# Optimization experiments

Measured on AMD Instinct MI355X. Metric: run time of the kernel, lower is better.

The kernel has to match this reference:

```python
import jax, jax.numpy as jnp
import numpy as np

NUM_GRAPHS = 512


def setup_inputs() -> dict:
    key = jax.random.key(0)
    k1, k2, k3, k4, k5, k6, k7 = jax.random.split(key, 7)
    N, E, D_IN, D_H = 100000, 3200000, 384, 64
    x_sem = jax.random.normal(k1, (N, D_IN), dtype=jnp.float32)
    edge_index = jax.random.randint(k2, (2, E), 0, N, dtype=jnp.int64)
    batch_index = jnp.sort(jax.random.randint(k3, (N,), 0, NUM_GRAPHS, dtype=jnp.int64))
    # GCNConv params: linear (no bias) + separate bias; classifier Linear(D_H, 1)
    W_gcn = jax.random.normal(k4, (D_IN, D_H), dtype=jnp.float32) / np.sqrt(D_IN)
    b_gcn = jnp.zeros((D_H,), dtype=jnp.float32)
    W_cls = jax.random.normal(k5, (D_H, 1), dtype=jnp.float32) / np.sqrt(D_H)
    b_cls = jnp.zeros((1,), dtype=jnp.float32)
    return {"x_sem": x_sem, "edge_index": edge_index, "batch_index": batch_index,
            "W_gcn": W_gcn, "b_gcn": b_gcn, "W_cls": W_cls, "b_cls": b_cls}


def reference(x_sem, edge_index, batch_index, W_gcn, b_gcn, W_cls, b_cls):
    N = x_sem.shape[0]
    # GCNConv: add self-loops, symmetric deg^{-1/2} A deg^{-1/2} normalization
    loop = jnp.arange(N, dtype=edge_index.dtype)
    src = jnp.concatenate([edge_index[0], loop])  # message source (x_j)
    dst = jnp.concatenate([edge_index[1], loop])  # aggregation target
    deg = jax.ops.segment_sum(jnp.ones_like(dst, dtype=x_sem.dtype), dst, num_segments=N)
    deg_inv_sqrt = jnp.where(deg > 0, jax.lax.rsqrt(jnp.maximum(deg, 1.0)), 0.0)
    norm = deg_inv_sqrt[src] * deg_inv_sqrt[dst]  # [E+N]
    h = x_sem @ W_gcn                                       # [N, D_H] project first (cheaper)
    msg = h[src] * norm[:, None]                            # gather + scale
    agg = jax.ops.segment_sum(msg, dst, num_segments=N) + b_gcn
    h = jax.nn.relu(agg)
    # global_add_pool over sorted batch_index
    z_graph = jax.ops.segment_sum(h, batch_index, num_segments=NUM_GRAPHS)  # [G, D_H]
    logits = z_graph @ W_cls + b_cls                        # [G, 1]
    return jnp.squeeze(logits, axis=-1)                     # [G]
```

## Files before the change

### kernel.cpp

```cpp
#include <hip/hip_runtime.h>
#include <hip/hip_bf16.h>

#define D_IN 384
#define D_H  64
#define BSH  7
#define BN   128
#define NBLK 512
#define EBUF 4608

typedef __attribute__((ext_vector_type(8))) short short8;
typedef __attribute__((ext_vector_type(4))) float f32x4;

__device__ __forceinline__ unsigned short f2bf(float f){
  unsigned u = __float_as_uint(f);
  u += 0x7fffu + ((u >> 16) & 1u);
  return (unsigned short)(u >> 16);
}
__device__ __forceinline__ float bf2f(unsigned short u){
  return __uint_as_float((unsigned)u << 16);
}

__global__ __launch_bounds__(256) void k_bcount2(const int* __restrict__ ei,
                                                 int* __restrict__ hists,
                                                 int E, int NB, int chunk){
  __shared__ int hist[1024];
  const int blk = blockIdx.x;
  const int t = threadIdx.x;
  for (int i = t; i < NB; i += 256) hist[i] = 0;
  __syncthreads();
  const int cs = blk * chunk;
  const int ce = min(E, cs + chunk);
  for (int e = cs + t; e < ce; e += 256)
    atomicAdd(&hist[ei[E + e] >> BSH], 1);
  __syncthreads();
  for (int i = t; i < NB; i += 256)
    hists[(size_t)blk * NB + i] = hist[i];
}

__global__ __launch_bounds__(NBLK) void k_blkscan(const int* __restrict__ hists,
                                                  int* __restrict__ offs,
                                                  int* __restrict__ bsum, int NB){
  __shared__ int sd[NBLK];
  const int b = blockIdx.x;
  const int t = threadIdx.x;
  int c = hists[(size_t)t * NB + b];
  sd[t] = c;
  __syncthreads();
  for (int off = 1; off < NBLK; off <<= 1){
    int v = (t >= off) ? sd[t - off] : 0;
    __syncthreads();
    sd[t] += v;
    __syncthreads();
  }
  offs[(size_t)b * NBLK + t] = sd[t] - c;
  if (t == NBLK - 1) bsum[b] = sd[t];
}

__global__ __launch_bounds__(1024) void k_bscan(const int* __restrict__ bsum,
                                                int* bstart, int NB, int E){
  __shared__ int sd[1024];
  int t = threadIdx.x;
  int c = (t < NB) ? bsum[t] : 0;
  sd[t] = c;
  __syncthreads();
  for (int off = 1; off < 1024; off <<= 1){
    int v = (t >= off) ? sd[t - off] : 0;
    __syncthreads();
    sd[t] += v;
    __syncthreads();
  }
  if (t < NB) bstart[t] = sd[t] - c;
  if (t == 0) bstart[NB] = E;
}

__global__ __launch_bounds__(256) void k_bscatter2(const int* __restrict__ ei,
                                                   const int* __restrict__ bstart,
                                                   const int* __restrict__ offs,
                                                   unsigned* __restrict__ bscat,
                                                   int E, int NB, int chunk){
  __shared__ int lcur[1024];
  const int blk = blockIdx.x;
  const int t = threadIdx.x;
  for (int i = t; i < NB; i += 256)
    lcur[i] = bstart[i] + offs[(size_t)i * NBLK + blk];
  __syncthreads();
  const int cs = blk * chunk;
  const int ce = min(E, cs + chunk);
  for (int e = cs + t; e < ce; e += 256){
    int s = ei[e];
    int d = ei[E + e];
    int b = d >> BSH;
    int pos = atomicAdd(&lcur[b], 1);
    bscat[pos] = ((unsigned)(d & (BN - 1)) << 17) | (unsigned)s;
  }
}

__global__ __launch_bounds__(256) void k_nodecsr(const unsigned* __restrict__ bscat,
                                                 const int* __restrict__ bstart,
                                                 int* __restrict__ csr,
                                                 int* __restrict__ rowstart,
                                                 float* __restrict__ dis,
                                                 int N, int NB, int E){
  __shared__ int lcnt[BN];
  __shared__ int sc[BN];
  __shared__ int lcur[BN];
  __shared__ unsigned ebuf[EBUF];
  const int b = blockIdx.x;
  const int t = threadIdx.x;
  const int es = bstart[b], ee = bstart[b + 1];
  const int cnt = ee - es;

  if (t < BN) lcnt[t] = 0;
  __syncthreads();
  for (int i = t; i < cnt; i += 256){
    unsigned p = bscat[es + i];
    if (i < EBUF) ebuf[i] = p;
    atomicAdd(&lcnt[p >> 17], 1);
  }
  __syncthreads();
  if (t < BN) sc[t] = lcnt[t];
  __syncthreads();
  for (int off = 1; off < BN; off <<= 1){
    int v = (t < BN && t >= off) ? sc[t - off] : 0;
    __syncthreads();
    if (t < BN) sc[t] += v;
    __syncthreads();
  }
  if (t < BN){
    int excl = sc[t] - lcnt[t];
    lcur[t] = excl;
    int node = b * BN + t;
    if (node < N){
      rowstart[node] = es + excl;
      dis[node] = rsqrtf((float)(lcnt[t] + 1));
    }
  }
  if (b == NB - 1 && t == 0) rowstart[N] = E;
  __syncthreads();
  for (int i = t; i < cnt; i += 256){
    unsigned p = (i < EBUF) ? ebuf[i] : bscat[es + i];
    int pos = atomicAdd(&lcur[p >> 17], 1);
    csr[es + pos] = (int)(p & 0x1FFFFu);
  }
}

__global__ __launch_bounds__(256) void k_gemm(const float* __restrict__ x,
                                              const float* __restrict__ W,
                                              const float* __restrict__ dis,
                                              unsigned short* __restrict__ hb, int N){
  __shared__ __align__(16) short a_sw[4 * 4 * 64 * 8];
  __shared__ __align__(16) short b_sw[4 * 4 * 64 * 8];
  const int t = threadIdx.x;
  const int node0 = blockIdx.x * 64;
  const int w = t >> 6;
  const int l = t & 63;

  f32x4 acc[4];
  #pragma unroll
  for (int nt = 0; nt < 4; nt++) acc[nt] = (f32x4){0.f, 0.f, 0.f, 0.f};

  for (int c = 0; c < 3; c++){
    const int kbase = c * 128;
    #pragma unroll
    for (int r = 0; r < 4; r++){
      int id  = t + 256 * r;
      int cl  = id & 63;
      int s   = (id >> 6) & 3;
      int tl  = id >> 8;
      int k   = kbase + s * 32 + ((cl >> 4) << 3);
      {
        int node = node0 + tl * 16 + (cl & 15);
        uint4 pv;
        if (node < N){
          const float* xp = &x[(size_t)node * D_IN + k];
          float4 u0 = *(const float4*)xp;
          float4 u1 = *(const float4*)(xp + 4);
          pv.x = (unsigned)f2bf(u0.x) | ((unsigned)f2bf(u0.y) << 16);
          pv.y = (unsigned)f2bf(u0.z) | ((unsigned)f2bf(u0.w) << 16);
          pv.z = (unsigned)f2bf(u1.x) | ((unsigned)f2bf(u1.y) << 16);
          pv.w = (unsigned)f2bf(u1.z) | ((unsigned)f2bf(u1.w) << 16);
        } else {
          pv.x = pv.y = pv.z = pv.w = 0u;
        }
        *reinterpret_cast<uint4*>(&a_sw[id * 8]) = pv;
      }
      {
        int n = tl * 16 + (cl & 15);
        const float* wp = &W[(size_t)k * D_H + n];
        uint4 qv;
        qv.x = (unsigned)f2bf(wp[0])   | ((unsigned)f2bf(wp[64])  << 16);
        qv.y = (unsigned)f2bf(wp[128]) | ((unsigned)f2bf(wp[192]) << 16);
        qv.z = (unsigned)f2bf(wp[256]) | ((unsigned)f2bf(wp[320]) << 16);
        qv.w = (unsigned)f2bf(wp[384]) | ((unsigned)f2bf(wp[448]) << 16);
        *reinterpret_cast<uint4*>(&b_sw[id * 8]) = qv;
      }
    }
    __syncthreads();
    #pragma unroll
    for (int s = 0; s < 4; s++){
      short8 a = *reinterpret_cast<const short8*>(&a_sw[((w * 4 + s) * 64 + l) * 8]);
      #pragma unroll
      for (int nt = 0; nt < 4; nt++){
        short8 b = *reinterpret_cast<const short8*>(&b_sw[((nt * 4 + s) * 64 + l) * 8]);
        acc[nt] = __builtin_amdgcn_mfma_f32_16x16x32_bf16(a, b, acc[nt], 0, 0, 0);
      }
    }
    __syncthreads();
  }
  const int qd = l >> 4;
  const int col0 = l & 15;
  #pragma unroll
  for (int r = 0; r < 4; r++){
    int node = node0 + w * 16 + qd * 4 + r;
    if (node < N){
      float scale = dis[node];
      #pragma unroll
      for (int nt = 0; nt < 4; nt++)
        hb[(size_t)node * D_H + nt * 16 + col0] = f2bf(acc[nt][r] * scale);
    }
  }
}

__global__ void k_agg(const unsigned short* __restrict__ hb,
                      const int* __restrict__ csr, const int* __restrict__ rowstart,
                      const float* __restrict__ dis, const float* __restrict__ bg,
                      float* __restrict__ hout, int N){
  int gid = blockIdx.x * blockDim.x + threadIdx.x;
  int i = gid >> 6;
  int f = gid & 63;
  if (i >= N) return;
  float acc = bf2f(hb[(size_t)i * D_H + f]);
  int rs = rowstart[i];
  int re = rowstart[i + 1];
  int e = rs;
  for (; e + 4 <= re; e += 4){
    int s0 = csr[e], s1 = csr[e + 1], s2 = csr[e + 2], s3 = csr[e + 3];
    float v0 = bf2f(hb[(size_t)s0 * D_H + f]);
    float v1 = bf2f(hb[(size_t)s1 * D_H + f]);
    float v2 = bf2f(hb[(size_t)s2 * D_H + f]);
    float v3 = bf2f(hb[(size_t)s3 * D_H + f]);
    acc += (v0 + v1) + (v2 + v3);
  }
  for (; e < re; e++)
    acc += bf2f(hb[(size_t)csr[e] * D_H + f]);
  float v = acc * dis[i] + bg[f];
  hout[(size_t)i * D_H + f] = v > 0.f ? v : 0.f;
}

__global__ void k_pool(const float* __restrict__ hout, const int* __restrict__ batch,
                       const float* __restrict__ wc, const float* __restrict__ bc,
                       float* __restrict__ out, int N, int G){
  int g = blockIdx.x;
  int t = threadIdx.x;
  int lo = 0, hi = N;
  while (lo < hi){ int m = (lo + hi) >> 1; if (batch[m] < g) lo = m + 1; else hi = m; }
  int start = lo;
  lo = start; hi = N;
  while (lo < hi){ int m = (lo + hi) >> 1; if (batch[m] < g + 1) lo = m + 1; else hi = m; }
  int end = lo;

  int f = t & 63;
  int r = t >> 6;
  float sum = 0.f;
  for (int i = start + r; i < end; i += 4) sum += hout[(size_t)i * D_H + f];
  __shared__ float red[256];
  red[t] = sum;
  __syncthreads();
  if (t < 64){
    float z = red[t] + red[t + 64] + red[t + 128] + red[t + 192];
    float p = z * wc[t];
    #pragma unroll
    for (int off = 32; off > 0; off >>= 1) p += __shfl_down(p, off);
    if (t == 0) out[g] = p + bc[0];
  }
}

extern "C" void kernel_launch(void* const* d_in, const int* in_sizes, int n_in,
                              void* d_out, int out_size, void* d_ws, size_t ws_size,
                              hipStream_t stream){
  const float* x     = (const float*)d_in[0];
  const int*   ei    = (const int*)d_in[1];
  const int*   batch = (const int*)d_in[2];
  const float* Wg    = (const float*)d_in[3];
  const float* bg    = (const float*)d_in[4];
  const float* wc    = (const float*)d_in[5];
  const float* bc    = (const float*)d_in[6];
  float* out = (float*)d_out;

  const int N = in_sizes[2];
  const int E = in_sizes[1] / 2;
  const int G = out_size;
  const int NB = (N + BN - 1) / BN;
  const int chunk = (E + NBLK - 1) / NBLK;

  char* ws = (char*)d_ws;
  size_t off = 0;
  auto alloc = [&](size_t bytes) -> void* {
    void* p = ws + off;
    off += (bytes + 255) & ~(size_t)255;
    return p;
  };
  int*            hists    = (int*)           alloc((size_t)NBLK * NB * 4);
  int*            offs     = (int*)           alloc((size_t)NB * NBLK * 4);
  int*            bsum     = (int*)           alloc((size_t)NB * 4);
  int*            bstart   = (int*)           alloc((size_t)(NB + 1) * 4);
  unsigned*       bscat    = (unsigned*)      alloc((size_t)E * 4);
  int*            csr      = (int*)           alloc((size_t)E * 4);
  int*            rowstart = (int*)           alloc((size_t)(N + 1) * 4);
  float*          dis      = (float*)         alloc((size_t)N * 4);
  unsigned short* hb       = (unsigned short*)alloc((size_t)N * D_H * 2);
  float*          hout     = (float*)         alloc((size_t)N * D_H * 4);

  k_bcount2  <<<NBLK, 256, 0, stream>>>(ei, hists, E, NB, chunk);
  k_blkscan  <<<NB, NBLK, 0, stream>>>(hists, offs, bsum, NB);
  k_bscan    <<<1, 1024, 0, stream>>>(bsum, bstart, NB, E);
  k_bscatter2<<<NBLK, 256, 0, stream>>>(ei, bstart, offs, bscat, E, NB, chunk);
  k_nodecsr  <<<NB, 256, 0, stream>>>(bscat, bstart, csr, rowstart, dis, N, NB, E);
  k_gemm     <<<(N + 63) / 64, 256, 0, stream>>>(x, Wg, dis, hb, N);
  k_agg      <<<(N + 3) / 4, 256, 0, stream>>>(hb, csr, rowstart, dis, bg, hout, N);
  k_pool     <<<G, 256, 0, stream>>>(hout, batch, wc, bc, out, N, G);
}
```

Measured before the change: 476.9 us.

## Pre-pack W to bf16 fragments, drop LDS in GEMM, vectorize aggregation gather

A new small kernel converts W_gcn once into the bf16 MFMA B-fragment layout, and k_gemm now reads its A fragments directly from global memory into registers, with no LDS staging and no barriers. The CSR stores pre-scaled byte offsets (node<<7). k_agg splits each wave into two half-waves that handle alternate edges, with each lane loading a packed bf16 pair, and the halves are combined with a shuffle. The aim is to cut LDS and sync overhead in the GEMM and to halve per-edge load instructions in the memory-bound gather, at the cost of uncoalesced-ish A loads and node indices limited to offsets that fit in int.

Result: faster. 439.9 us (-7.8%).

```diff
diff --git a/kernel.cpp b/kernel.cpp
--- a/kernel.cpp
+++ b/kernel.cpp
@@ -11,10 +11,10 @@
 typedef __attribute__((ext_vector_type(8))) short short8;
 typedef __attribute__((ext_vector_type(4))) float f32x4;
 
-__device__ __forceinline__ unsigned short f2bf(float f){
+__device__ __forceinline__ unsigned f2bf(float f){
   unsigned u = __float_as_uint(f);
   u += 0x7fffu + ((u >> 16) & 1u);
-  return (unsigned short)(u >> 16);
+  return u >> 16;
 }
 __device__ __forceinline__ float bf2f(unsigned short u){
   return __uint_as_float((unsigned)u << 16);
@@ -140,72 +140,61 @@
   for (int i = t; i < cnt; i += 256){
     unsigned p = (i < EBUF) ? ebuf[i] : bscat[es + i];
     int pos = atomicAdd(&lcur[p >> 17], 1);
-    csr[es + pos] = (int)(p & 0x1FFFFu);
-  }
+    csr[es + pos] = (int)((p & 0x1FFFFu) << 7);
+  }
+}
+
+__global__ void k_wconv(const float* __restrict__ W, uint4* __restrict__ bpre){
+  int j = blockIdx.x * blockDim.x + threadIdx.x;
+  if (j >= 3072) return;
+  int id = j & 1023, c = j >> 10;
+  int cl = id & 63, s = (id >> 6) & 3, tl = id >> 8;
+  int k = c * 128 + s * 32 + ((cl >> 4) << 3);
+  int n = tl * 16 + (cl & 15);
+  const float* wp = &W[(size_t)k * D_H + n];
+  uint4 qv;
+  qv.x = f2bf(wp[0])   | (f2bf(wp[64])  << 16);
+  qv.y = f2bf(wp[128]) | (f2bf(wp[192]) << 16);
+  qv.z = f2bf(wp[256]) | (f2bf(wp[320]) << 16);
+  qv.w = f2bf(wp[384]) | (f2bf(wp[448]) << 16);
+  bpre[j] = qv;
 }
 
 __global__ __launch_bounds__(256) void k_gemm(const float* __restrict__ x,
-                                              const float* __restrict__ W,
+                                              const uint4* __restrict__ bpre,
                                               const float* __restrict__ dis,
                                               unsigned short* __restrict__ hb, int N){
-  __shared__ __align__(16) short a_sw[4 * 4 * 64 * 8];
-  __shared__ __align__(16) short b_sw[4 * 4 * 64 * 8];
-  const int t = threadIdx.x;
-  const int node0 = blockIdx.x * 64;
+  const int t = threadIdx.x;
   const int w = t >> 6;
   const int l = t & 63;
+  const int node0 = blockIdx.x * 64;
+  const int row = node0 + w * 16 + (l & 15);
+  const int rowc = row < N ? row : N - 1;
+  const float* xr = x + (size_t)rowc * D_IN + ((l >> 4) << 3);
 
   f32x4 acc[4];
   #pragma unroll
   for (int nt = 0; nt < 4; nt++) acc[nt] = (f32x4){0.f, 0.f, 0.f, 0.f};
 
+  #pragma unroll
   for (int c = 0; c < 3; c++){
-    const int kbase = c * 128;
-    #pragma unroll
-    for (int r = 0; r < 4; r++){
-      int id  = t + 256 * r;
-      int cl  = id & 63;
-      int s   = (id >> 6) & 3;
-      int tl  = id >> 8;
-      int k   = kbase + s * 32 + ((cl >> 4) << 3);
-      {
-        int node = node0 + tl * 16 + (cl & 15);
-        uint4 pv;
-        if (node < N){
-          const float* xp = &x[(size_t)node * D_IN + k];
-          float4 u0 = *(const float4*)xp;
-          float4 u1 = *(const float4*)(xp + 4);
-          pv.x = (unsigned)f2bf(u0.x) | ((unsigned)f2bf(u0.y) << 16);
-          pv.y = (unsigned)f2bf(u0.z) | ((unsigned)f2bf(u0.w) << 16);
-          pv.z = (unsigned)f2bf(u1.x) | ((unsigned)f2bf(u1.y) << 16);
-          pv.w = (unsigned)f2bf(u1.z) | ((unsigned)f2bf(u1.w) << 16);
-        } else {
-          pv.x = pv.y = pv.z = pv.w = 0u;
-        }
-        *reinterpret_cast<uint4*>(&a_sw[id * 8]) = pv;
-      }
-      {
-        int n = tl * 16 + (cl & 15);
-        const float* wp = &W[(size_t)k * D_H + n];
-        uint4 qv;
-        qv.x = (unsigned)f2bf(wp[0])   | ((unsigned)f2bf(wp[64])  << 16);
-        qv.y = (unsigned)f2bf(wp[128]) | ((unsigned)f2bf(wp[192]) << 16);
-        qv.z = (unsigned)f2bf(wp[256]) | ((unsigned)f2bf(wp[320]) << 16);
-        qv.w = (unsigned)f2bf(wp[384]) | ((unsigned)f2bf(wp[448]) << 16);
-        *reinterpret_cast<uint4*>(&b_sw[id * 8]) = qv;
-      }
-    }
-    __syncthreads();
     #pragma unroll
     for (int s = 0; s < 4; s++){
-      short8 a = *reinterpret_cast<const short8*>(&a_sw[((w * 4 + s) * 64 + l) * 8]);
+      const float* xp = xr + c * 128 + s * 32;
+      float4 u0 = *(const float4*)xp;
+      float4 u1 = *(const float4*)(xp + 4);
+      uint4 pv;
+      pv.x = f2bf(u0.x) | (f2bf(u0.y) << 16);
+      pv.y = f2bf(u0.z) | (f2bf(u0.w) << 16);
+      pv.z = f2bf(u1.x) | (f2bf(u1.y) << 16);
+      pv.w = f2bf(u1.z) | (f2bf(u1.w) << 16);
+      short8 a = *reinterpret_cast<short8*>(&pv);
       #pragma unroll
       for (int nt = 0; nt < 4; nt++){
-        short8 b = *reinterpret_cast<const short8*>(&b_sw[((nt * 4 + s) * 64 + l) * 8]);
+        short8 b = *reinterpret_cast<const short8*>(&bpre[c * 1024 + (nt * 4 + s) * 64 + l]);
         acc[nt] = __builtin_amdgcn_mfma_f32_16x16x32_bf16(a, b, acc[nt], 0, 0, 0);
       }
     }
-    __syncthreads();
   }
   const int qd = l >> 4;
   const int col0 = l & 15;
@@ -216,35 +205,73 @@
       float scale = dis[node];
       #pragma unroll
       for (int nt = 0; nt < 4; nt++)
-        hb[(size_t)node * D_H + nt * 16 + col0] = f2bf(acc[nt][r] * scale);
-    }
-  }
-}
-
-__global__ void k_agg(const unsigned short* __restrict__ hb,
-                      const int* __restrict__ csr, const int* __restrict__ rowstart,
-                      const float* __restrict__ dis, const float* __restrict__ bg,
-                      float* __restrict__ hout, int N){
-  int gid = blockIdx.x * blockDim.x + threadIdx.x;
-  int i = gid >> 6;
-  int f = gid & 63;
+        hb[(size_t)node * D_H + nt * 16 + col0] = (unsigned short)f2bf(acc[nt][r] * scale);
+    }
+  }
+}
+
+__global__ __launch_bounds__(256) void k_agg(const unsigned short* __restrict__ hb,
+                                             const int* __restrict__ csr,
+                                             const int* __restrict__ rowstart,
+                                             const float* __restrict__ dis,
+                                             const float* __restrict__ bg,
+                                             float* __restrict__ hout, int N){
+  int gid = blockIdx.x * 256 + (int)threadIdx.x;
+  int i = __builtin_amdgcn_readfirstlane(gid >> 6);
   if (i >= N) return;
-  float acc = bf2f(hb[(size_t)i * D_H + f]);
-  int rs = rowstart[i];
-  int re = rowstart[i + 1];
-  int e = rs;
-  for (; e + 4 <= re; e += 4){
-    int s0 = csr[e], s1 = csr[e + 1], s2 = csr[e + 2], s3 = csr[e + 3];
-    float v0 = bf2f(hb[(size_t)s0 * D_H + f]);
-    float v1 = bf2f(hb[(size_t)s1 * D_H + f]);
-    float v2 = bf2f(hb[(size_t)s2 * D_H + f]);
-    float v3 = bf2f(hb[(size_t)s3 * D_H + f]);
-    acc += (v0 + v1) + (v2 + v3);
-  }
-  for (; e < re; e++)
-    acc += bf2f(hb[(size_t)csr[e] * D_H + f]);
-  float v = acc * dis[i] + bg[f];
-  hout[(size_t)i * D_H + f] = v > 0.f ? v : 0.f;
+  const int l = threadIdx.x & 63;
+  const int c4 = (l & 31) << 2;
+  const int hsel = l >> 5;
+  const char* hbb = (const char*)hb;
+  float ax = 0.f, ay = 0.f;
+
+  {
+    unsigned u = *(const unsigned*)(hbb + ((size_t)(unsigned)i << 7) + c4);
+    if (!hsel){
+      ax += __uint_as_float(u << 16);
+      ay += __uint_as_float(u & 0xffff0000u);
+    }
+  }
+  int e = rowstart[i];
+  const int re = rowstart[i + 1];
+  for (; e + 8 <= re; e += 8){
+    int b0 = csr[e + 0], b1 = csr[e + 1];
+    int b2 = csr[e + 2], b3 = csr[e + 3];
+    int b4 = csr[e + 4], b5 = csr[e + 5];
+    int b6 = csr[e + 6], b7 = csr[e + 7];
+    unsigned u0 = *(const unsigned*)(hbb + (size_t)(unsigned)(hsel ? b1 : b0) + c4);
+    unsigned u1 = *(const unsigned*)(hbb + (size_t)(unsigned)(hsel ? b3 : b2) + c4);
+    unsigned u2 = *(const unsigned*)(hbb + (size_t)(unsigned)(hsel ? b5 : b4) + c4);
+    unsigned u3 = *(const unsigned*)(hbb + (size_t)(unsigned)(hsel ? b7 : b6) + c4);
+    ax += __uint_as_float(u0 << 16);          ay += __uint_as_float(u0 & 0xffff0000u);
+    ax += __uint_as_float(u1 << 16);          ay += __uint_as_float(u1 & 0xffff0000u);
+    ax += __uint_as_float(u2 << 16);          ay += __uint_as_float(u2 & 0xffff0000u);
+    ax += __uint_as_float(u3 << 16);          ay += __uint_as_float(u3 & 0xffff0000u);
+  }
+  for (; e + 2 <= re; e += 2){
+    int b0 = csr[e], b1 = csr[e + 1];
+    unsigned u = *(const unsigned*)(hbb + (size_t)(unsigned)(hsel ? b1 : b0) + c4);
+    ax += __uint_as_float(u << 16);
+    ay += __uint_as_float(u & 0xffff0000u);
+  }
+  if (e < re){
+    int b0 = csr[e];
+    unsigned u = *(const unsigned*)(hbb + (size_t)(unsigned)b0 + c4);
+    if (!hsel){
+      ax += __uint_as_float(u << 16);
+      ay += __uint_as_float(u & 0xffff0000u);
+    }
+  }
+  ax += __shfl_xor(ax, 32);
+  ay += __shfl_xor(ay, 32);
+  if (!hsel){
+    float di = dis[i];
+    float2 bb = *(const float2*)(bg + (c4 >> 1));
+    float vx = ax * di + bb.x; vx = vx > 0.f ? vx : 0.f;
+    float vy = ay * di + bb.y; vy = vy > 0.f ? vy : 0.f;
+    float2 o = make_float2(vx, vy);
+    *(float2*)((char*)hout + (((size_t)(unsigned)i) << 8) + (c4 << 1)) = o;
+  }
 }
 
 __global__ void k_pool(const float* __restrict__ hout, const int* __restrict__ batch,
@@ -308,15 +335,17 @@
   int*            csr      = (int*)           alloc((size_t)E * 4);
   int*            rowstart = (int*)           alloc((size_t)(N + 1) * 4);
   float*          dis      = (float*)         alloc((size_t)N * 4);
+  uint4*          bpre     = (uint4*)         alloc((size_t)3072 * 16);
   unsigned short* hb       = (unsigned short*)alloc((size_t)N * D_H * 2);
   float*          hout     = (float*)         alloc((size_t)N * D_H * 4);
 
+  k_wconv    <<<12, 256, 0, stream>>>(Wg, bpre);
   k_bcount2  <<<NBLK, 256, 0, stream>>>(ei, hists, E, NB, chunk);
   k_blkscan  <<<NB, NBLK, 0, stream>>>(hists, offs, bsum, NB);
   k_bscan    <<<1, 1024, 0, stream>>>(bsum, bstart, NB, E);
   k_bscatter2<<<NBLK, 256, 0, stream>>>(ei, bstart, offs, bscat, E, NB, chunk);
   k_nodecsr  <<<NB, 256, 0, stream>>>(bscat, bstart, csr, rowstart, dis, N, NB, E);
-  k_gemm     <<<(N + 63) / 64, 256, 0, stream>>>(x, Wg, dis, hb, N);
+  k_gemm     <<<(N + 63) / 64, 256, 0, stream>>>(x, bpre, dis, hb, N);
   k_agg      <<<(N + 3) / 4, 256, 0, stream>>>(hb, csr, rowstart, dis, bg, hout, N);
   k_pool     <<<G, 256, 0, stream>>>(hout, batch, wc, bc, out, N, G);
 }
```
